# Optimization experiments

Measured on AMD Instinct MI355X. Metric: run time of the kernel, lower is better.

The kernel has to match this reference:

```python
import jax, jax.numpy as jnp
import numpy as np

TEMPERATURE = 8.0  # sqrt(head_dim=64)
NEG_BIG = -10000.0


def setup_inputs() -> dict:
    key = jax.random.key(0)
    kq, kk, kv, km = jax.random.split(key, 4)
    B, H, S, D, K = 4, 8, 1024, 64, 4
    q = jax.random.normal(kq, (B, H, S, D), dtype=jnp.float32)
    k = jax.random.normal(kk, (B, H, S, D), dtype=jnp.float32)
    v = jax.random.normal(kv, (B, H, S, D), dtype=jnp.float32)
    # K binary attention masks, broadcastable to [B,H,S,S]
    mask = jax.random.randint(km, (K, 1, 1, S, S), 0, 2).astype(jnp.float32)
    return {"q": q, "k": k, "v": v, "mask": mask}


def reference(q, k, v, mask):
    # attn: [B,H,S,S]
    attn = jnp.einsum("bhsd,bhtd->bhst", q / TEMPERATURE, k)
    # additive mask: [K,1,1,S,S]
    ext_mask = (1.0 - mask) * NEG_BIG
    # batched over K instead of the original python loop: [K,B,H,S,S]
    probs = jax.nn.softmax(attn[None] + ext_mask, axis=-1)
    # dropout is identity in eval mode (deterministic reference)
    output = jnp.einsum("kbhst,bhtd->kbhsd", probs, v)
    return (output, attn)
```

## Files before the change

### kernel.cpp

```cpp
#include <hip/hip_runtime.h>
#include <hip/hip_bf16.h>
#include <stdint.h>

typedef float f4 __attribute__((ext_vector_type(4)));
typedef short bf8 __attribute__((ext_vector_type(8)));
typedef uint32_t u4 __attribute__((ext_vector_type(4)));
typedef uint32_t u2 __attribute__((ext_vector_type(2)));

#define SDIM 1024
#define DDIM 64
#define NBH  32
#define KM   4
#define NT   16

#define MB_BLK 4096
#define KB_BLK 1024
#define VT_BLK 512

__device__ __forceinline__ unsigned short f2bf(float f) {
  uint32_t u = __builtin_bit_cast(uint32_t, f);
  u += 0x7fffu + ((u >> 16) & 1u);
  return (unsigned short)(u >> 16);
}

#define GLOAD16(gsrc, ldst)                                                  \
  __builtin_amdgcn_global_load_lds(                                          \
      (const __attribute__((address_space(1))) unsigned int*)(gsrc),         \
      (__attribute__((address_space(3))) unsigned int*)(ldst), 16, 0, 0)

__device__ __forceinline__ bf8 lds_ld(const unsigned short* base, int row, int e0) {
  return *(const bf8*)((const char*)base + (((row * 64 + e0) * 2) ^ ((row & 7) << 4)));
}

__global__ __launch_bounds__(256) void prepass(
    const float* __restrict__ k, const float* __restrict__ v,
    const float* __restrict__ mask, unsigned short* __restrict__ kb,
    unsigned short* __restrict__ vt, uint32_t* __restrict__ mb2) {
  __shared__ float tv[64][65];
  const int b = blockIdx.x;
  const int t = threadIdx.x;
  if (b < MB_BLK) {
    int gid4 = (b * 256 + t) * 4;
    f4 x = *(const f4*)(mask + gid4);
    uint32_t bits = (x[0] > 0.5f ? 1u : 0u) | (x[1] > 0.5f ? 2u : 0u) |
                    (x[2] > 0.5f ? 4u : 0u) | (x[3] > 0.5f ? 8u : 0u);
    uint32_t wv = bits << (gid4 & 28);
    wv |= __shfl_xor(wv, 1);
    wv |= __shfl_xor(wv, 2);
    wv |= __shfl_xor(wv, 4);
    if ((t & 7) == 0) {
      int m = gid4 >> 20;
      int r = (gid4 >> 10) & 1023;
      int c = gid4 & 1023;
      mb2[m * 32768 + (c >> 5) * 1024 + r] = wv;
    }
  } else if (b < MB_BLK + KB_BLK) {
    int base = ((b - MB_BLK) * 256 + t) * 8;
    f4 a = *(const f4*)(k + base);
    f4 c = *(const f4*)(k + base + 4);
    bf8 o;
    o[0] = (short)f2bf(a[0]); o[1] = (short)f2bf(a[1]);
    o[2] = (short)f2bf(a[2]); o[3] = (short)f2bf(a[3]);
    o[4] = (short)f2bf(c[0]); o[5] = (short)f2bf(c[1]);
    o[6] = (short)f2bf(c[2]); o[7] = (short)f2bf(c[3]);
    *(bf8*)(kb + base) = o;
  } else {
    int vb = b - MB_BLK - KB_BLK;
    int bh = vb >> 4;
    int s0 = (vb & 15) * 64;
    int sr = t >> 2, c0 = (t & 3) * 16;
    const float* vp = v + ((size_t)(bh * SDIM) + s0 + sr) * DDIM + c0;
#pragma unroll
    for (int i = 0; i < 4; ++i) {
      f4 x = *(const f4*)(vp + 4 * i);
#pragma unroll
      for (int j = 0; j < 4; ++j) tv[sr][c0 + 4 * i + j] = x[j];
    }
    __syncthreads();
    int d = t >> 2, sc0 = (t & 3) * 16;
    unsigned short tmp[16];
#pragma unroll
    for (int i = 0; i < 16; ++i) tmp[i] = f2bf(tv[sc0 + i][d]);
    unsigned short* op = vt + ((size_t)(bh * DDIM) + d) * SDIM + s0 + sc0;
    bf8 o0, o1;
#pragma unroll
    for (int j = 0; j < 8; ++j) { o0[j] = (short)tmp[j]; o1[j] = (short)tmp[j + 8]; }
    *(bf8*)(op) = o0;
    *(bf8*)(op + 8) = o1;
  }
}

__global__ __launch_bounds__(256, 4) void attn_main(
    const float* __restrict__ qf, const unsigned short* __restrict__ kb,
    const unsigned short* __restrict__ vtg, const uint32_t* __restrict__ mb2,
    float* __restrict__ outO, float* __restrict__ attn) {
  __shared__ __align__(16) unsigned short k_s0[64 * 64];
  __shared__ __align__(16) unsigned short k_s1[64 * 64];
  __shared__ __align__(16) unsigned short v_s0[64 * 64];
  __shared__ __align__(16) unsigned short v_s1[64 * 64];
  __shared__ __align__(16) unsigned short e_s[32 * 64];

  const int tid = threadIdx.x;
  const int l   = tid & 63;
  const int w   = tid >> 6;
  const int l16 = l & 15;
  const int lg  = l >> 4;
  const int wh  = w & 1;
  const int wc  = w >> 1;

  int bid = (int)blockIdx.x;
  bid = (bid & 7) * 128 + (bid >> 3);
  const int bh = bid >> 5;
  const int r0 = (bid & 31) * 32;

  const int srow = tid >> 3;
  const int sd   = ((tid & 7) ^ (srow & 7)) << 3;
  const unsigned short* ksrc0 = kb  + ((size_t)(bh * SDIM) + srow) * DDIM + sd;
  const unsigned short* ksrc1 = kb  + ((size_t)(bh * SDIM) + srow + 32) * DDIM + sd;
  const unsigned short* vsrc0 = vtg + ((size_t)(bh * DDIM) + srow) * SDIM + sd;
  const unsigned short* vsrc1 = vtg + ((size_t)(bh * DDIM) + srow + 32) * SDIM + sd;

  GLOAD16(ksrc0, k_s0 + tid * 8);
  GLOAD16(ksrc1, k_s0 + (tid + 256) * 8);
  GLOAD16(vsrc0, v_s0 + tid * 8);
  GLOAD16(vsrc1, v_s0 + (tid + 256) * 8);

  bf8 bq0, bq1;
  {
    const float* qp = qf + ((size_t)(bh * SDIM) + r0 + 16 * wh + l16) * DDIM + lg * 8;
    f4 a0 = *(const f4*)qp;
    f4 a1 = *(const f4*)(qp + 4);
    f4 a2 = *(const f4*)(qp + 32);
    f4 a3 = *(const f4*)(qp + 36);
#pragma unroll
    for (int j = 0; j < 4; ++j) {
      bq0[j]     = (short)f2bf(a0[j] * 0.125f);
      bq0[j + 4] = (short)f2bf(a1[j] * 0.125f);
      bq1[j]     = (short)f2bf(a2[j] * 0.125f);
      bq1[j + 4] = (short)f2bf(a3[j] * 0.125f);
    }
  }

  f4 acc[2][4] = {};
  f4 accl[2]   = {};
  bf8 ones;
#pragma unroll
  for (int b = 0; b < 8; ++b) ones[b] = (short)0x3F80;

  const uint32_t* mbase = mb2 + w * 32768 + r0 + l16;

  uint32_t mdwA[2][2], mdwB[2][2];
#pragma unroll
  for (int mt2 = 0; mt2 < 2; ++mt2)
#pragma unroll
    for (int kt = 0; kt < 2; ++kt)
      mdwA[mt2][kt] = mbase[kt * 1024 + 16 * mt2];

  __syncthreads();

#define BODY(CT, KR, VR, KW, VW, MR, MW, PF)                                   \
  {                                                                            \
    if (PF) {                                                                  \
      GLOAD16(ksrc0 + (size_t)((CT) + 1) * 4096, (KW) + tid * 8);              \
      GLOAD16(ksrc1 + (size_t)((CT) + 1) * 4096, (KW) + (tid + 256) * 8);      \
      GLOAD16(vsrc0 + (size_t)((CT) + 1) * 64, (VW) + tid * 8);                \
      GLOAD16(vsrc1 + (size_t)((CT) + 1) * 64, (VW) + (tid + 256) * 8);        \
    }                                                                          \
    {                                                                          \
      const int kc0 = 32 * wc + l16;                                           \
      bf8 ak0 = lds_ld((KR), kc0, lg * 8);                                     \
      bf8 ak1 = lds_ld((KR), kc0, lg * 8 + 32);                                \
      bf8 ak2 = lds_ld((KR), kc0 + 16, lg * 8);                                \
      bf8 ak3 = lds_ld((KR), kc0 + 16, lg * 8 + 32);                           \
      f4 s0 = {}, s1 = {};                                                     \
      s0 = __builtin_amdgcn_mfma_f32_16x16x32_bf16(ak0, bq0, s0, 0, 0, 0);     \
      s0 = __builtin_amdgcn_mfma_f32_16x16x32_bf16(ak1, bq1, s0, 0, 0, 0);     \
      s1 = __builtin_amdgcn_mfma_f32_16x16x32_bf16(ak2, bq0, s1, 0, 0, 0);     \
      s1 = __builtin_amdgcn_mfma_f32_16x16x32_bf16(ak3, bq1, s1, 0, 0, 0);     \
      float* arow = attn + ((size_t)(bh * SDIM) + r0 + 16 * wh + l16) * SDIM   \
                    + (CT) * 64 + 32 * wc + 4 * lg;                            \
      *(f4*)(arow) = s0;                                                       \
      *(f4*)(arow + 16) = s1;                                                  \
      const int erow = 16 * wh + l16;                                          \
      u2 ev0, ev1;                                                             \
      ev0[0] = (uint32_t)f2bf(__expf(s0[0])) | ((uint32_t)f2bf(__expf(s0[1])) << 16); \
      ev0[1] = (uint32_t)f2bf(__expf(s0[2])) | ((uint32_t)f2bf(__expf(s0[3])) << 16); \
      ev1[0] = (uint32_t)f2bf(__expf(s1[0])) | ((uint32_t)f2bf(__expf(s1[1])) << 16); \
      ev1[1] = (uint32_t)f2bf(__expf(s1[2])) | ((uint32_t)f2bf(__expf(s1[3])) << 16); \
      const int colA = 32 * wc + 4 * lg;                                       \
      *(u2*)((char*)e_s + (((erow * 64 + colA) * 2) ^ ((erow & 7) << 4))) = ev0; \
      *(u2*)((char*)e_s + (((erow * 64 + colA + 16) * 2) ^ ((erow & 7) << 4))) = ev1; \
    }                                                                          \
    asm volatile("s_waitcnt lgkmcnt(0)\n\ts_barrier" ::: "memory");            \
    {                                                                          \
      bf8 af[2][2];                                                            \
      _Pragma("unroll") for (int mt2 = 0; mt2 < 2; ++mt2) {                    \
        const int row = 16 * mt2 + l16;                                        \
        _Pragma("unroll") for (int kt = 0; kt < 2; ++kt) {                     \
          bf8 e = lds_ld(e_s, row, kt * 32 + lg * 8);                          \
          uint32_t bits = ((MR)[mt2][kt] >> (lg * 8)) & 0xffu;                 \
          u4 ew = __builtin_bit_cast(u4, e);                                   \
          _Pragma("unroll") for (int d = 0; d < 4; ++d) {                      \
            uint32_t n2 = (bits >> (2 * d)) & 3u;                              \
            uint32_t sp = (n2 * 0x8001u) & 0x00010001u;                        \
            ew[d] &= (sp << 16) - sp;                                          \
          }                                                                    \
          af[mt2][kt] = __builtin_bit_cast(bf8, ew);                           \
        }                                                                      \
        accl[mt2] = __builtin_amdgcn_mfma_f32_16x16x32_bf16(af[mt2][0], ones, accl[mt2], 0, 0, 0); \
        accl[mt2] = __builtin_amdgcn_mfma_f32_16x16x32_bf16(af[mt2][1], ones, accl[mt2], 0, 0, 0); \
      }                                                                        \
      _Pragma("unroll") for (int nt = 0; nt < 4; ++nt) {                       \
        const int dc = 16 * nt + l16;                                          \
        bf8 bv0 = lds_ld((VR), dc, lg * 8);                                    \
        bf8 bv1 = lds_ld((VR), dc, lg * 8 + 32);                               \
        _Pragma("unroll") for (int mt2 = 0; mt2 < 2; ++mt2) {                  \
          acc[mt2][nt] = __builtin_amdgcn_mfma_f32_16x16x32_bf16(af[mt2][0], bv0, acc[mt2][nt], 0, 0, 0); \
          acc[mt2][nt] = __builtin_amdgcn_mfma_f32_16x16x32_bf16(af[mt2][1], bv1, acc[mt2][nt], 0, 0, 0); \
        }                                                                      \
      }                                                                        \
    }                                                                          \
    if (PF) {                                                                  \
      _Pragma("unroll") for (int mt2 = 0; mt2 < 2; ++mt2)                      \
        _Pragma("unroll") for (int kt = 0; kt < 2; ++kt)                       \
          (MW)[mt2][kt] = mbase[(((CT) + 1) * 2 + kt) * 1024 + 16 * mt2];      \
    }                                                                          \
    __syncthreads();                                                           \
  }

  for (int ct2 = 0; ct2 < NT / 2; ++ct2) {
    BODY(2 * ct2,     k_s0, v_s0, k_s1, v_s1, mdwA, mdwB, true);
    BODY(2 * ct2 + 1, k_s1, v_s1, k_s0, v_s0, mdwB, mdwA, (ct2 < NT / 2 - 1));
  }
#undef BODY

#pragma unroll
  for (int mt2 = 0; mt2 < 2; ++mt2) {
#pragma unroll
    for (int r = 0; r < 4; ++r) {
      float inv = 1.0f / accl[mt2][r];
      int row = 16 * mt2 + 4 * lg + r;
      float* orow = outO + (((size_t)(w * NBH + bh)) * SDIM + r0 + row) * DDIM + l16;
#pragma unroll
      for (int nt = 0; nt < 4; ++nt)
        orow[16 * nt] = acc[mt2][nt][r] * inv;
    }
  }
}

extern "C" void kernel_launch(void* const* d_in, const int* in_sizes, int n_in,
                              void* d_out, int out_size, void* d_ws, size_t ws_size,
                              hipStream_t stream) {
  (void)in_sizes; (void)n_in; (void)out_size; (void)ws_size;
  const float* q    = (const float*)d_in[0];
  const float* k    = (const float*)d_in[1];
  const float* v    = (const float*)d_in[2];
  const float* mask = (const float*)d_in[3];
  float* outO = (float*)d_out;
  float* attn = (float*)d_out + (size_t)KM * NBH * SDIM * DDIM;

  char* ws = (char*)d_ws;
  unsigned short* kb = (unsigned short*)ws;
  unsigned short* vt = (unsigned short*)(ws + (4u << 20));
  uint32_t*       mb = (uint32_t*)(ws + (8u << 20));

  prepass<<<MB_BLK + KB_BLK + VT_BLK, 256, 0, stream>>>(k, v, mask, kb, vt, mb);
  attn_main<<<NBH * 32, 256, 0, stream>>>(q, kb, vt, mb, outO, attn);
}
```

Baseline: 54.74 us.

## Double query rows per block to 64 with 512 threads to halve K/V staging

Each block now covers 64 query rows using 8 waves instead of 32 rows with 4 waves, and the grid shrinks from 1024 to 512 blocks. Each K/V tile loaded into LDS is therefore reused by twice as many query rows, which halves global and LDS staging traffic per output. Waves are remapped: the row tile comes from w>>1 and selects the mask, and the column half comes from w&1. The risks are fewer blocks, which may underfill the GPU (512 blocks on 256 CUs), and barriers that now synchronise 8 waves.

```diff
diff --git a/kernel.cpp b/kernel.cpp
--- a/kernel.cpp
+++ b/kernel.cpp
@@ -90,7 +90,7 @@
   }
 }
 
-__global__ __launch_bounds__(256, 4) void attn_main(
+__global__ __launch_bounds__(512, 4) void attn_main(
     const float* __restrict__ qf, const unsigned short* __restrict__ kb,
     const unsigned short* __restrict__ vtg, const uint32_t* __restrict__ mb2,
     float* __restrict__ outO, float* __restrict__ attn) {
@@ -98,36 +98,32 @@
   __shared__ __align__(16) unsigned short k_s1[64 * 64];
   __shared__ __align__(16) unsigned short v_s0[64 * 64];
   __shared__ __align__(16) unsigned short v_s1[64 * 64];
-  __shared__ __align__(16) unsigned short e_s[32 * 64];
+  __shared__ __align__(16) unsigned short e_s[64 * 64];
 
   const int tid = threadIdx.x;
   const int l   = tid & 63;
   const int w   = tid >> 6;
   const int l16 = l & 15;
   const int lg  = l >> 4;
-  const int wh  = w & 1;
-  const int wc  = w >> 1;
+  const int rt  = w >> 1;
+  const int cp  = w & 1;
 
   int bid = (int)blockIdx.x;
-  bid = (bid & 7) * 128 + (bid >> 3);
-  const int bh = bid >> 5;
-  const int r0 = (bid & 31) * 32;
+  bid = (bid & 7) * 64 + (bid >> 3);
+  const int bh = bid >> 4;
+  const int r0 = (bid & 15) * 64;
 
   const int srow = tid >> 3;
   const int sd   = ((tid & 7) ^ (srow & 7)) << 3;
-  const unsigned short* ksrc0 = kb  + ((size_t)(bh * SDIM) + srow) * DDIM + sd;
-  const unsigned short* ksrc1 = kb  + ((size_t)(bh * SDIM) + srow + 32) * DDIM + sd;
-  const unsigned short* vsrc0 = vtg + ((size_t)(bh * DDIM) + srow) * SDIM + sd;
-  const unsigned short* vsrc1 = vtg + ((size_t)(bh * DDIM) + srow + 32) * SDIM + sd;
-
-  GLOAD16(ksrc0, k_s0 + tid * 8);
-  GLOAD16(ksrc1, k_s0 + (tid + 256) * 8);
-  GLOAD16(vsrc0, v_s0 + tid * 8);
-  GLOAD16(vsrc1, v_s0 + (tid + 256) * 8);
+  const unsigned short* ksrc = kb  + ((size_t)(bh * SDIM) + srow) * DDIM + sd;
+  const unsigned short* vsrc = vtg + ((size_t)(bh * DDIM) + srow) * SDIM + sd;
+
+  GLOAD16(ksrc, k_s0 + tid * 8);
+  GLOAD16(vsrc, v_s0 + tid * 8);
 
   bf8 bq0, bq1;
   {
-    const float* qp = qf + ((size_t)(bh * SDIM) + r0 + 16 * wh + l16) * DDIM + lg * 8;
+    const float* qp = qf + ((size_t)(bh * SDIM) + r0 + 16 * rt + l16) * DDIM + lg * 8;
     f4 a0 = *(const f4*)qp;
     f4 a1 = *(const f4*)(qp + 4);
     f4 a2 = *(const f4*)(qp + 32);
@@ -147,27 +143,25 @@
 #pragma unroll
   for (int b = 0; b < 8; ++b) ones[b] = (short)0x3F80;
 
-  const uint32_t* mbase = mb2 + w * 32768 + r0 + l16;
+  const uint32_t* mbase = mb2 + rt * 32768 + r0 + l16;
 
   uint32_t mdwA[2][2], mdwB[2][2];
 #pragma unroll
   for (int mt2 = 0; mt2 < 2; ++mt2)
 #pragma unroll
     for (int kt = 0; kt < 2; ++kt)
-      mdwA[mt2][kt] = mbase[kt * 1024 + 16 * mt2];
+      mdwA[mt2][kt] = mbase[kt * 1024 + 32 * cp + 16 * mt2];
 
   __syncthreads();
 
 #define BODY(CT, KR, VR, KW, VW, MR, MW, PF)                                   \
   {                                                                            \
     if (PF) {                                                                  \
-      GLOAD16(ksrc0 + (size_t)((CT) + 1) * 4096, (KW) + tid * 8);              \
-      GLOAD16(ksrc1 + (size_t)((CT) + 1) * 4096, (KW) + (tid + 256) * 8);      \
-      GLOAD16(vsrc0 + (size_t)((CT) + 1) * 64, (VW) + tid * 8);                \
-      GLOAD16(vsrc1 + (size_t)((CT) + 1) * 64, (VW) + (tid + 256) * 8);        \
+      GLOAD16(ksrc + (size_t)((CT) + 1) * 4096, (KW) + tid * 8);               \
+      GLOAD16(vsrc + (size_t)((CT) + 1) * 64, (VW) + tid * 8);                 \
     }                                                                          \
     {                                                                          \
-      const int kc0 = 32 * wc + l16;                                           \
+      const int kc0 = 32 * cp + l16;                                           \
       bf8 ak0 = lds_ld((KR), kc0, lg * 8);                                     \
       bf8 ak1 = lds_ld((KR), kc0, lg * 8 + 32);                                \
       bf8 ak2 = lds_ld((KR), kc0 + 16, lg * 8);                                \
@@ -177,17 +171,17 @@
       s0 = __builtin_amdgcn_mfma_f32_16x16x32_bf16(ak1, bq1, s0, 0, 0, 0);     \
       s1 = __builtin_amdgcn_mfma_f32_16x16x32_bf16(ak2, bq0, s1, 0, 0, 0);     \
       s1 = __builtin_amdgcn_mfma_f32_16x16x32_bf16(ak3, bq1, s1, 0, 0, 0);     \
-      float* arow = attn + ((size_t)(bh * SDIM) + r0 + 16 * wh + l16) * SDIM   \
-                    + (CT) * 64 + 32 * wc + 4 * lg;                            \
+      float* arow = attn + ((size_t)(bh * SDIM) + r0 + 16 * rt + l16) * SDIM   \
+                    + (CT) * 64 + 32 * cp + 4 * lg;                            \
       *(f4*)(arow) = s0;                                                       \
       *(f4*)(arow + 16) = s1;                                                  \
-      const int erow = 16 * wh + l16;                                          \
+      const int erow = 16 * rt + l16;                                          \
       u2 ev0, ev1;                                                             \
       ev0[0] = (uint32_t)f2bf(__expf(s0[0])) | ((uint32_t)f2bf(__expf(s0[1])) << 16); \
       ev0[1] = (uint32_t)f2bf(__expf(s0[2])) | ((uint32_t)f2bf(__expf(s0[3])) << 16); \
       ev1[0] = (uint32_t)f2bf(__expf(s1[0])) | ((uint32_t)f2bf(__expf(s1[1])) << 16); \
       ev1[1] = (uint32_t)f2bf(__expf(s1[2])) | ((uint32_t)f2bf(__expf(s1[3])) << 16); \
-      const int colA = 32 * wc + 4 * lg;                                       \
+      const int colA = 32 * cp + 4 * lg;                                       \
       *(u2*)((char*)e_s + (((erow * 64 + colA) * 2) ^ ((erow & 7) << 4))) = ev0; \
       *(u2*)((char*)e_s + (((erow * 64 + colA + 16) * 2) ^ ((erow & 7) << 4))) = ev1; \
     }                                                                          \
@@ -195,7 +189,7 @@
     {                                                                          \
       bf8 af[2][2];                                                            \
       _Pragma("unroll") for (int mt2 = 0; mt2 < 2; ++mt2) {                    \
-        const int row = 16 * mt2 + l16;                                        \
+        const int row = 32 * cp + 16 * mt2 + l16;                              \
         _Pragma("unroll") for (int kt = 0; kt < 2; ++kt) {                     \
           bf8 e = lds_ld(e_s, row, kt * 32 + lg * 8);                          \
           uint32_t bits = ((MR)[mt2][kt] >> (lg * 8)) & 0xffu;                 \
@@ -223,7 +217,7 @@
     if (PF) {                                                                  \
       _Pragma("unroll") for (int mt2 = 0; mt2 < 2; ++mt2)                      \
         _Pragma("unroll") for (int kt = 0; kt < 2; ++kt)                       \
-          (MW)[mt2][kt] = mbase[(((CT) + 1) * 2 + kt) * 1024 + 16 * mt2];      \
+          (MW)[mt2][kt] = mbase[(((CT) + 1) * 2 + kt) * 1024 + 32 * cp + 16 * mt2]; \
     }                                                                          \
     __syncthreads();                                                           \
   }
@@ -239,8 +233,8 @@
 #pragma unroll
     for (int r = 0; r < 4; ++r) {
       float inv = 1.0f / accl[mt2][r];
-      int row = 16 * mt2 + 4 * lg + r;
-      float* orow = outO + (((size_t)(w * NBH + bh)) * SDIM + r0 + row) * DDIM + l16;
+      int row = 32 * cp + 16 * mt2 + 4 * lg + r;
+      float* orow = outO + (((size_t)(rt * NBH + bh)) * SDIM + r0 + row) * DDIM + l16;
 #pragma unroll
       for (int nt = 0; nt < 4; ++nt)
         orow[16 * nt] = acc[mt2][nt][r] * inv;
@@ -265,5 +259,5 @@
   uint32_t*       mb = (uint32_t*)(ws + (8u << 20));
 
   prepass<<<MB_BLK + KB_BLK + VT_BLK, 256, 0, stream>>>(k, v, mask, kb, vt, mb);
-  attn_main<<<NBH * 32, 256, 0, stream>>>(q, kb, vt, mb, outO, attn);
-}
+  attn_main<<<NBH * 16, 512, 0, stream>>>(q, kb, vt, mb, outO, attn);
+}
```

Result: no change. 54.48 us, median of 2 (-0.5%).
